# Kernel tuning notes

Hardware: AMD Instinct MI355X
Metric: run time of the kernel (lower is better)

The kernel has to match this reference:

```python
import jax, jax.numpy as jnp
import numpy as np
import math

B, M, DM = 4, 4096, 1024
H, HD = 16, 64            # head_dim = hidden_dim // num_heads
SEG, DIL = 128, 2         # segment_size, dilation_rate
BLOCK_M = 64              # kernel query-block size (min(64, M))
SCALE = HD ** -0.5


def _hilbert_map(seq_len):
    # Faithful port of create_hilbert_mapping_fixed (boustrophedon scan).
    if seq_len <= 64:
        return np.arange(seq_len, dtype=np.int32)
    g = int(math.ceil(math.sqrt(seq_len)))
    mp = np.zeros(seq_len, dtype=np.int64)
    idx = 0
    for row in range(g):
        cols = range(g) if row % 2 == 0 else range(g - 1, -1, -1)
        for col in cols:
            if idx < seq_len:
                lp = row * g + col
                if lp < seq_len:
                    mp[lp] = idx
                    idx += 1
    for i in range(seq_len):
        if i >= idx:
            mp[i] = i
    return mp.astype(np.int32)


def setup_inputs() -> dict:
    key = jax.random.key(0)
    k1, k2, k3 = jax.random.split(key, 3)
    x = jax.random.normal(k1, (B, M, DM), jnp.float32)
    Wqkv = jax.random.normal(k2, (3 * DM, DM), jnp.float32) * 0.02
    Wout = jax.random.normal(k3, (DM, DM), jnp.float32) * 0.02
    hmap = jnp.asarray(_hilbert_map(M))
    return {"x": x, "Wqkv": Wqkv, "Wout": Wout, "hmap": hmap}


def _hilbert_attention(x, Wqkv, Wout, hmap):
    Bn, Mn, _ = x.shape
    qkv = x @ Wqkv.T                                   # [B,M,3*DM]
    qkv = qkv.reshape(Bn, Mn, 3, H, HD).transpose(2, 0, 3, 1, 4)
    q, k, v = qkv[0], qkv[1], qkv[2]                   # [B,H,M,HD]

    S = Mn // SEG           # number of segments
    T = SEG // DIL          # keys per segment (dilated offsets 0, DIL, 2*DIL, ...)
    NB = SEG // BLOCK_M     # query blocks per segment

    # Queries gathered through Hilbert map, pre-scaled (as in kernel).
    qh = q[:, :, hmap, :] * SCALE                      # [B,H,M,HD]

    # Dilated key positions per segment, gathered through Hilbert map.
    key_pos = (jnp.arange(S)[:, None] * SEG + jnp.arange(T)[None, :] * DIL).reshape(-1)
    kh = k[:, :, hmap[key_pos], :].reshape(Bn, H, S, T, HD)
    vh = v[:, :, hmap[key_pos], :].reshape(Bn, H, S, T, HD)

    # Scores per (query-block within segment, key): [B,H,S,NB,BLOCK_M,T]
    qs = qh.reshape(Bn, H, S, NB, BLOCK_M, HD)
    scores = jnp.einsum('bhsnqd,bhstd->bhsnqt', qs, kh)

    # Kernel quirk (faithful): per-KEY max taken over the 64-query block,
    # exp accumulated without rescaling -> NOT a true softmax.
    c = jnp.max(scores, axis=4, keepdims=True)         # max over query block
    w = jnp.exp(scores - c)
    num = jnp.einsum('bhsnqt,bhstd->bhsnqd', w, vh)
    den = 1e-10 + jnp.sum(w, axis=-1, keepdims=True)
    out = (num / den).reshape(Bn, H, Mn, HD)

    # Stored at linear (non-Hilbert) positions, then merged heads + out proj.
    out = out.transpose(0, 2, 1, 3).reshape(Bn, Mn, H * HD)
    return out @ Wout.T


def reference(x, Wqkv, Wout, hmap):
    return _hilbert_attention(x, Wqkv, Wout, hmap)
```

## Files before the change

kernel.cpp:

```cpp
#include <hip/hip_runtime.h>
#include <hip/hip_bf16.h>

#define BB 4
#define MM 4096
#define DM 1024
#define NH 16
#define HDIM 64
#define SEGSZ 128
#define NSEG 32
#define ROWS (BB*MM)
#define QKVC (3*DM)
#define KVROWS (BB*MM/2)
#define KVLD 2048
#define NX4  (ROWS*DM/4)
#define NW14 (QKVC*DM/4)
#define NW24 (DM*DM/4)

typedef __attribute__((ext_vector_type(8))) short bf16x8;
typedef __attribute__((ext_vector_type(4))) float f32x4;

__device__ inline unsigned short f2bf(float f) {
  __hip_bfloat16 h = __float2bfloat16(f);
  return *reinterpret_cast<unsigned short*>(&h);
}

__device__ __forceinline__ void gld16(const ushort* g, ushort* l) {
  __builtin_amdgcn_global_load_lds(
      (const __attribute__((address_space(1))) unsigned int*)g,
      (__attribute__((address_space(3))) unsigned int*)l,
      16, 0, 0);
}

__global__ __launch_bounds__(256) void cvt_all(const float4* __restrict__ x,
                                               const float4* __restrict__ w1,
                                               const float4* __restrict__ w2,
                                               ushort4* __restrict__ xo,
                                               ushort4* __restrict__ w1o,
                                               ushort4* __restrict__ w2o) {
  int i = blockIdx.x * 256 + threadIdx.x;
  const float4* src; ushort4* dst; int off;
  if (i < NX4)              { src = x;  dst = xo;  off = i; }
  else if (i < NX4 + NW14)  { src = w1; dst = w1o; off = i - NX4; }
  else                      { src = w2; dst = w2o; off = i - NX4 - NW14; }
  float4 v = src[off];
  ushort4 o;
  o.x = f2bf(v.x); o.y = f2bf(v.y); o.z = f2bf(v.z); o.w = f2bf(v.w);
  dst[off] = o;
}

#define STAGE_AB(T, KH, DB) do {                                             \
    gld16(pA0 + (T) * 64 + (KH) * 32,                                        \
          sAB + ((DB) * 2 + (KH)) * 8192 + wave * 512);                      \
    gld16(pA1 + (T) * 64 + (KH) * 32,                                        \
          sAB + ((DB) * 2 + (KH)) * 8192 + 4096 + wave * 512);               \
    gld16(pB0 + (T) * 64 + (KH) * 32,                                        \
          sAB + 32768 + ((DB) * 2 + (KH)) * 8192 + wave * 512);              \
    gld16(pB1 + (T) * 64 + (KH) * 32,                                        \
          sAB + 32768 + ((DB) * 2 + (KH)) * 8192 + 4096 + wave * 512);       \
  } while (0)
#define VM4 asm volatile("s_waitcnt vmcnt(4)" ::: "memory")
#define VM0 asm volatile("s_waitcnt vmcnt(0)" ::: "memory")
#define NOPS ((void)0)

#define PH_M(TB, KH, STAGE, VMA) do {                                        \
    const ushort* Ab = sAB + ((TB) * 2 + (KH)) * 8192;                       \
    const ushort* Bb = sAB + 32768 + ((TB) * 2 + (KH)) * 8192;               \
    _Pragma("unroll")                                                        \
    for (int mf = 0; mf < 8; ++mf) {                                         \
      int r = wm * 128 + mf * 16 + m16;                                      \
      af[mf] = *(const bf16x8*)(Ab + r * 32 + ((quad ^ ((r >> 1) & 3)) << 3)); \
    }                                                                        \
    _Pragma("unroll")                                                        \
    for (int nf = 0; nf < 4; ++nf) {                                         \
      int r = wn * 64 + nf * 16 + m16;                                       \
      bfv[nf] = *(const bf16x8*)(Bb + r * 32 + ((quad ^ ((r >> 1) & 3)) << 3)); \
    }                                                                        \
    STAGE; VMA;                                                              \
    __builtin_amdgcn_s_barrier();                                            \
    __builtin_amdgcn_s_setprio(1);                                           \
    _Pragma("unroll")                                                        \
    for (int mf = 0; mf < 8; ++mf)                                           \
      _Pragma("unroll")                                                      \
      for (int nf = 0; nf < 4; ++nf)                                         \
        acc[mf][nf] = __builtin_amdgcn_mfma_f32_16x16x32_bf16(               \
            af[mf], bfv[nf], acc[mf][nf], 0, 0, 0);                          \
    __builtin_amdgcn_s_setprio(0);                                           \
  } while (0)

#define KLOOP_1024                                                           \
  STAGE_AB(0, 0, 0);                                                         \
  STAGE_AB(0, 1, 0);                                                         \
  VM4;                                                                       \
  __builtin_amdgcn_s_barrier();                                              \
  _Pragma("unroll 1")                                                        \
  for (int i = 0; i < 7; ++i) {                                              \
    const int t1 = 2 * i + 1, t2 = 2 * i + 2;                                \
    PH_M(0, 0, STAGE_AB(t1, 0, 1), VM4);                                     \
    PH_M(0, 1, STAGE_AB(t1, 1, 1), VM4);                                     \
    PH_M(1, 0, STAGE_AB(t2, 0, 0), VM4);                                     \
    PH_M(1, 1, STAGE_AB(t2, 1, 0), VM4);                                     \
  }                                                                          \
  PH_M(0, 0, STAGE_AB(15, 0, 1), VM4);                                       \
  PH_M(0, 1, STAGE_AB(15, 1, 1), VM4);                                       \
  PH_M(1, 0, NOPS, VM0);                                                     \
  PH_M(1, 1, NOPS, NOPS);

__global__ __launch_bounds__(512) void gemm_qkv(const ushort* __restrict__ xbf,
                                                const ushort* __restrict__ wqkv,
                                                ushort* __restrict__ qhb,
                                                ushort* __restrict__ kvb,
                                                const int* __restrict__ hmap) {
  __shared__ __align__(16) ushort sAB[65536];
  __shared__ int sRow[256];

  const int blk = blockIdx.x;
  const int tid = threadIdx.x;
  const int lane = tid & 63;
  const int wave = tid >> 6;
  const int m16 = lane & 15;
  const int quad = lane >> 4;
  const int wm = wave >> 2;
  const int wn = wave & 3;

  const int j0 = blk & 255;
  const int swz = (j0 & 7) * 32 + (j0 >> 3);

  const ushort* Bmat; ushort* C; int row0, col0, N;
  if (blk < 256) {
    row0 = (swz >> 2) * 256; col0 = (swz & 3) * 256;
    Bmat = wqkv; C = qhb; N = DM;
  } else {
    row0 = (swz >> 3) * 256; col0 = (swz & 7) * 256;
    Bmat = wqkv + (size_t)DM * DM; C = kvb; N = KVLD;
  }

  if (tid < 256) {
    int m = row0 + tid, xrow;
    if (blk < 256) {
      int b = m >> 12, p = m & 4095;
      xrow = (b << 12) + hmap[p];
    } else {
      int b = m >> 11, idx = m & 2047;
      int ss = idx >> 6, tt = idx & 63;
      xrow = (b << 12) + hmap[ss * SEGSZ + 2 * tt];
    }
    sRow[tid] = xrow;
  }
  __syncthreads();

  const int f0 = wave * 64 + lane, f1 = 512 + f0;
  const int r0 = f0 >> 2, c0 = (f0 & 3) ^ ((f0 >> 3) & 3);
  const int r1 = f1 >> 2, c1 = (f1 & 3) ^ ((f1 >> 3) & 3);
  const ushort* pA0 = xbf + (size_t)sRow[r0] * DM + c0 * 8;
  const ushort* pA1 = xbf + (size_t)sRow[r1] * DM + c1 * 8;
  const ushort* pB0 = Bmat + (size_t)(col0 + r0) * DM + c0 * 8;
  const ushort* pB1 = Bmat + (size_t)(col0 + r1) * DM + c1 * 8;

  f32x4 acc[8][4] = {};
  bf16x8 af[8], bfv[4];

  KLOOP_1024

#pragma unroll
  for (int mf = 0; mf < 8; ++mf)
#pragma unroll
    for (int rr = 0; rr < 4; ++rr) {
      int row = row0 + wm * 128 + mf * 16 + quad * 4 + rr;
#pragma unroll
      for (int nf = 0; nf < 4; ++nf)
        C[(size_t)row * N + col0 + wn * 64 + nf * 16 + m16] = f2bf(acc[mf][nf][rr]);
    }
}

__global__ __launch_bounds__(512) void gemm_out(const ushort* __restrict__ A,
                                                const ushort* __restrict__ Bmat,
                                                float* __restrict__ C) {
  __shared__ __align__(16) ushort sAB[65536];

  const int tid = threadIdx.x;
  const int lane = tid & 63;
  const int wave = tid >> 6;
  const int m16 = lane & 15;
  const int quad = lane >> 4;
  const int wm = wave >> 2;
  const int wn = wave & 3;

  const int j0 = blockIdx.x;
  const int swz = (j0 & 7) * 32 + (j0 >> 3);
  const int row0 = (swz >> 2) * 256;
  const int col0 = (swz & 3) * 256;

  const int f0 = wave * 64 + lane, f1 = 512 + f0;
  const int r0 = f0 >> 2, c0 = (f0 & 3) ^ ((f0 >> 3) & 3);
  const int r1 = f1 >> 2, c1 = (f1 & 3) ^ ((f1 >> 3) & 3);
  const ushort* pA0 = A + (size_t)(row0 + r0) * DM + c0 * 8;
  const ushort* pA1 = A + (size_t)(row0 + r1) * DM + c1 * 8;
  const ushort* pB0 = Bmat + (size_t)(col0 + r0) * DM + c0 * 8;
  const ushort* pB1 = Bmat + (size_t)(col0 + r1) * DM + c1 * 8;

  f32x4 acc[8][4] = {};
  bf16x8 af[8], bfv[4];

  KLOOP_1024

#pragma unroll
  for (int mf = 0; mf < 8; ++mf)
#pragma unroll
    for (int rr = 0; rr < 4; ++rr) {
      int row = row0 + wm * 128 + mf * 16 + quad * 4 + rr;
#pragma unroll
      for (int nf = 0; nf < 4; ++nf)
        C[(size_t)row * DM + col0 + wn * 64 + nf * 16 + m16] = acc[mf][nf][rr];
    }
}

#undef KLOOP_1024
#undef PH_M
#undef STAGE_AB
#undef VM4
#undef VM0
#undef NOPS

__global__ __launch_bounds__(256) void attn_kernel(const ushort* __restrict__ qh,
                                                   const ushort* __restrict__ kv,
                                                   ushort* __restrict__ out) {
  __shared__ __align__(16) ushort sQW[128 * 72];
  __shared__ __align__(16) ushort sK[64 * 72];
  __shared__ __align__(16) ushort sVT[64 * 72];
  __shared__ float sCmaxW[4 * 64];
  __shared__ float sDen[128];

  const int bid = blockIdx.x;
  const int s  = bid & 31;
  const int h  = (bid >> 5) & 15;
  const int b  = bid >> 9;
  const int tid = threadIdx.x;
  const int lane = tid & 63;
  const int wave = tid >> 6;
  const int m16 = lane & 15;
  const int quad = lane >> 4;
  const int qb = wave * 32;
  const int hb = wave >> 1;

  {
    const int qr = tid >> 1;
    const int qc = (tid & 1) * 32;
    const ushort* qrow = qh + (size_t)(b * MM + s * SEGSZ + qr) * DM + h * HDIM + qc;
    *(uint4*)(sQW + qr * 72 + qc)      = ((const uint4*)qrow)[0];
    *(uint4*)(sQW + qr * 72 + qc + 8)  = ((const uint4*)qrow)[1];
    *(uint4*)(sQW + qr * 72 + qc + 16) = ((const uint4*)qrow)[2];
    *(uint4*)(sQW + qr * 72 + qc + 24) = ((const uint4*)qrow)[3];

    const int r = tid >> 2;
    const int c = (tid & 3) * 16;
    const ushort* krow = kv + (size_t)(b * (MM/2) + s * 64 + r) * KVLD + h * HDIM + c;
    const ushort* vrow = krow + DM;
    *(uint4*)(sK + r * 72 + c)     = ((const uint4*)krow)[0];
    *(uint4*)(sK + r * 72 + c + 8) = ((const uint4*)krow)[1];
    ushort vv[16];
    *(uint4*)(vv)     = ((const uint4*)vrow)[0];
    *(uint4*)(vv + 8) = ((const uint4*)vrow)[1];
#pragma unroll
    for (int u = 0; u < 16; ++u) sVT[(c + u) * 72 + r] = vv[u];
  }
  __syncthreads();

  f32x4 sc[2][4];
  {
    bf16x8 aq[2][2], bk[4][2];
#pragma unroll
    for (int ks = 0; ks < 2; ++ks) {
#pragma unroll
      for (int ib = 0; ib < 2; ++ib)
        aq[ib][ks] = *(const bf16x8*)(sQW + (qb + ib * 16 + m16) * 72 + ks * 32 + quad * 8);
#pragma unroll
      for (int j = 0; j < 4; ++j)
        bk[j][ks] = *(const bf16x8*)(sK + (j * 16 + m16) * 72 + ks * 32 + quad * 8);
    }
#pragma unroll
    for (int ib = 0; ib < 2; ++ib)
#pragma unroll
      for (int j = 0; j < 4; ++j) {
        f32x4 a = {};
        a = __builtin_amdgcn_mfma_f32_16x16x32_bf16(aq[ib][0], bk[j][0], a, 0, 0, 0);
        a = __builtin_amdgcn_mfma_f32_16x16x32_bf16(aq[ib][1], bk[j][1], a, 0, 0, 0);
        sc[ib][j] = a * 0.125f;
      }
  }

#pragma unroll
  for (int j = 0; j < 4; ++j) {
    float m = -1e30f;
#pragma unroll
    for (int ib = 0; ib < 2; ++ib)
#pragma unroll
      for (int r = 0; r < 4; ++r) m = fmaxf(m, sc[ib][j][r]);
    m = fmaxf(m, __shfl_xor(m, 16));
    m = fmaxf(m, __shfl_xor(m, 32));
    if (quad == 0) sCmaxW[wave * 64 + j * 16 + m16] = m;
  }
  __syncthreads();

  {
    float part[2][4] = {};
#pragma unroll
    for (int j = 0; j < 4; ++j) {
      const int col = j * 16 + m16;
      float c0 = fmaxf(sCmaxW[hb * 128 + col], sCmaxW[hb * 128 + 64 + col]);
#pragma unroll
      for (int ib = 0; ib < 2; ++ib)
#pragma unroll
        for (int r = 0; r < 4; ++r) {
          float ww = __expf(sc[ib][j][r] - c0);
          sc[ib][j][r] = ww;
          part[ib][r] += ww;
        }
    }
#pragma unroll
    for (int ib = 0; ib < 2; ++ib)
#pragma unroll
      for (int r = 0; r < 4; ++r) {
        float p = part[ib][r];
        p += __shfl_xor(p, 1); p += __shfl_xor(p, 2);
        p += __shfl_xor(p, 4); p += __shfl_xor(p, 8);
        if (m16 == 0) sDen[qb + ib * 16 + quad * 4 + r] = p;
      }
#pragma unroll
    for (int ib = 0; ib < 2; ++ib)
#pragma unroll
      for (int j = 0; j < 4; ++j)
#pragma unroll
        for (int r = 0; r < 4; ++r)
          sQW[(qb + ib * 16 + quad * 4 + r) * 72 + j * 16 + m16] = f2bf(sc[ib][j][r]);
  }
  __syncthreads();

  f32x4 o[2][4] = {};
  {
    bf16x8 aw[2][2], bv[4][2];
#pragma unroll
    for (int ks = 0; ks < 2; ++ks) {
#pragma unroll
      for (int ib = 0; ib < 2; ++ib)
        aw[ib][ks] = *(const bf16x8*)(sQW + (qb + ib * 16 + m16) * 72 + ks * 32 + quad * 8);
#pragma unroll
      for (int j = 0; j < 4; ++j)
        bv[j][ks] = *(const bf16x8*)(sVT + (j * 16 + m16) * 72 + ks * 32 + quad * 8);
    }
#pragma unroll
    for (int ib = 0; ib < 2; ++ib)
#pragma unroll
      for (int j = 0; j < 4; ++j) {
        o[ib][j] = __builtin_amdgcn_mfma_f32_16x16x32_bf16(aw[ib][0], bv[j][0], o[ib][j], 0, 0, 0);
        o[ib][j] = __builtin_amdgcn_mfma_f32_16x16x32_bf16(aw[ib][1], bv[j][1], o[ib][j], 0, 0, 0);
      }
  }

#pragma unroll
  for (int ib = 0; ib < 2; ++ib)
#pragma unroll
    for (int r = 0; r < 4; ++r) {
      const int lrow = qb + ib * 16 + quad * 4 + r;
      float rd = 1.0f / (1e-10f + sDen[lrow]);
      ushort* op = out + (size_t)(b * MM + s * SEGSZ + lrow) * DM + h * HDIM + m16;
#pragma unroll
      for (int j = 0; j < 4; ++j)
        op[j * 16] = f2bf(o[ib][j][r] * rd);
    }
}

extern "C" void kernel_launch(void* const* d_in, const int* in_sizes, int n_in,
                              void* d_out, int out_size, void* d_ws, size_t ws_size,
                              hipStream_t stream) {
  const float* x    = (const float*)d_in[0];
  const float* wqkv = (const float*)d_in[1];
  const float* wout = (const float*)d_in[2];
  const int*   hmap = (const int*)d_in[3];
  float* outp = (float*)d_out;

  ushort* xbf    = (ushort*)d_ws;
  ushort* wqkvbf = xbf + (size_t)ROWS * DM;
  ushort* woutbf = wqkvbf + (size_t)QKVC * DM;
  ushort* qhb    = woutbf + (size_t)DM * DM;
  ushort* kvb    = qhb + (size_t)ROWS * DM;
  ushort* attn   = kvb + (size_t)KVROWS * KVLD;

  cvt_all<<<(NX4 + NW14 + NW24 + 255) / 256, 256, 0, stream>>>(
      (const float4*)x, (const float4*)wqkv, (const float4*)wout,
      (ushort4*)xbf, (ushort4*)wqkvbf, (ushort4*)woutbf);

  gemm_qkv<<<512, 512, 0, stream>>>(xbf, wqkvbf, qhb, kvb, hmap);

  attn_kernel<<<BB * NH * NSEG, 256, 0, stream>>>(qhb, kvb, attn);

  gemm_out<<<256, 512, 0, stream>>>(attn, woutbf, outp);
}
```

Measured before the change: 252.2 us.

## Split QKV GEMM phases into half-N sub-phases with deeper prefetch pipeline

The QKV projection GEMM main loop now splits each k-phase into two half-width sub-phases, each issuing half of the B fragment loads and half the MFMAs, with A and B global-to-LDS staging interleaved separately. Prefetch runs three stages ahead instead of two, with finer vmcnt waits. The goal is to overlap memory latency better and reduce register pressure (bfv shrinks from 4 to 2 fragments). In exchange there are twice as many barriers per k-step and A fragments are reused across sub-phases. The output GEMM keeps the original schedule under renamed macros.

```diff
diff --git a/kernel.cpp b/kernel.cpp
--- a/kernel.cpp
+++ b/kernel.cpp
@@ -48,62 +48,93 @@
   dst[off] = o;
 }
 
-#define STAGE_AB(T, KH, DB) do {                                             \
+#define QSTAGE_A(T, KH, DB) do {                                             \
     gld16(pA0 + (T) * 64 + (KH) * 32,                                        \
           sAB + ((DB) * 2 + (KH)) * 8192 + wave * 512);                      \
     gld16(pA1 + (T) * 64 + (KH) * 32,                                        \
           sAB + ((DB) * 2 + (KH)) * 8192 + 4096 + wave * 512);               \
+  } while (0)
+#define QSTAGE_B(T, KH, DB) do {                                             \
     gld16(pB0 + (T) * 64 + (KH) * 32,                                        \
           sAB + 32768 + ((DB) * 2 + (KH)) * 8192 + wave * 512);              \
     gld16(pB1 + (T) * 64 + (KH) * 32,                                        \
           sAB + 32768 + ((DB) * 2 + (KH)) * 8192 + 4096 + wave * 512);       \
   } while (0)
-#define VM4 asm volatile("s_waitcnt vmcnt(4)" ::: "memory")
-#define VM0 asm volatile("s_waitcnt vmcnt(0)" ::: "memory")
-#define NOPS ((void)0)
-
-#define PH_M(TB, KH, STAGE, VMA) do {                                        \
-    const ushort* Ab = sAB + ((TB) * 2 + (KH)) * 8192;                       \
-    const ushort* Bb = sAB + 32768 + ((TB) * 2 + (KH)) * 8192;               \
+#define QVM6 asm volatile("s_waitcnt vmcnt(6)" ::: "memory")
+#define QVM8 asm volatile("s_waitcnt vmcnt(8)" ::: "memory")
+#define QVM0 asm volatile("s_waitcnt vmcnt(0)" ::: "memory")
+#define QNOPS ((void)0)
+
+#define QPH_TAIL(CH)                                                         \
+    __builtin_amdgcn_s_barrier();                                            \
+    __builtin_amdgcn_s_setprio(1);                                           \
+    _Pragma("unroll")                                                        \
+    for (int mf = 0; mf < 8; ++mf)                                           \
+      _Pragma("unroll")                                                      \
+      for (int nf = 0; nf < 2; ++nf)                                         \
+        acc[mf][(CH) * 2 + nf] = __builtin_amdgcn_mfma_f32_16x16x32_bf16(    \
+            af[mf], bfv[nf], acc[mf][(CH) * 2 + nf], 0, 0, 0);               \
+    __builtin_amdgcn_s_setprio(0);
+
+#define QPH_F_B(AB, BB_, STAGE, VMA) do {                                    \
+    const ushort* Ab = (AB); const ushort* Bb = (BB_);                       \
     _Pragma("unroll")                                                        \
     for (int mf = 0; mf < 8; ++mf) {                                         \
       int r = wm * 128 + mf * 16 + m16;                                      \
       af[mf] = *(const bf16x8*)(Ab + r * 32 + ((quad ^ ((r >> 1) & 3)) << 3)); \
     }                                                                        \
     _Pragma("unroll")                                                        \
-    for (int nf = 0; nf < 4; ++nf) {                                         \
+    for (int nf = 0; nf < 2; ++nf) {                                         \
       int r = wn * 64 + nf * 16 + m16;                                       \
       bfv[nf] = *(const bf16x8*)(Bb + r * 32 + ((quad ^ ((r >> 1) & 3)) << 3)); \
     }                                                                        \
     STAGE; VMA;                                                              \
-    __builtin_amdgcn_s_barrier();                                            \
-    __builtin_amdgcn_s_setprio(1);                                           \
-    _Pragma("unroll")                                                        \
-    for (int mf = 0; mf < 8; ++mf)                                           \
-      _Pragma("unroll")                                                      \
-      for (int nf = 0; nf < 4; ++nf)                                         \
-        acc[mf][nf] = __builtin_amdgcn_mfma_f32_16x16x32_bf16(               \
-            af[mf], bfv[nf], acc[mf][nf], 0, 0, 0);                          \
-    __builtin_amdgcn_s_setprio(0);                                           \
-  } while (0)
-
-#define KLOOP_1024                                                           \
-  STAGE_AB(0, 0, 0);                                                         \
-  STAGE_AB(0, 1, 0);                                                         \
-  VM4;                                                                       \
+    QPH_TAIL(0)                                                              \
+  } while (0)
+
+#define QPH_L_B(BB_, STAGE, VMA) do {                                        \
+    const ushort* Bb = (BB_);                                                \
+    _Pragma("unroll")                                                        \
+    for (int nf = 0; nf < 2; ++nf) {                                         \
+      int r = wn * 64 + 32 + nf * 16 + m16;                                  \
+      bfv[nf] = *(const bf16x8*)(Bb + r * 32 + ((quad ^ ((r >> 1) & 3)) << 3)); \
+    }                                                                        \
+    STAGE; VMA;                                                              \
+    QPH_TAIL(1)                                                              \
+  } while (0)
+
+#define QPH_F(TB, KH, STAGE, VMA) \
+    QPH_F_B(sAB + ((TB) * 2 + (KH)) * 8192, sAB + 32768 + ((TB) * 2 + (KH)) * 8192, STAGE, VMA)
+#define QPH_L(TB, KH, STAGE, VMA) \
+    QPH_L_B(sAB + 32768 + ((TB) * 2 + (KH)) * 8192, STAGE, VMA)
+
+#define QKLOOP_1024                                                          \
+  QSTAGE_A(0, 0, 0); QSTAGE_B(0, 0, 0);                                      \
+  QSTAGE_A(0, 1, 0); QSTAGE_B(0, 1, 0);                                      \
+  QSTAGE_A(1, 0, 1); QSTAGE_B(1, 0, 1);                                      \
+  QVM8;                                                                      \
   __builtin_amdgcn_s_barrier();                                              \
   _Pragma("unroll 1")                                                        \
   for (int i = 0; i < 7; ++i) {                                              \
-    const int t1 = 2 * i + 1, t2 = 2 * i + 2;                                \
-    PH_M(0, 0, STAGE_AB(t1, 0, 1), VM4);                                     \
-    PH_M(0, 1, STAGE_AB(t1, 1, 1), VM4);                                     \
-    PH_M(1, 0, STAGE_AB(t2, 0, 0), VM4);                                     \
-    PH_M(1, 1, STAGE_AB(t2, 1, 0), VM4);                                     \
+    const int t1 = 2 * i + 1, t2 = 2 * i + 2, t3 = 2 * i + 3;                \
+    QPH_F(0, 0, QSTAGE_A(t1, 1, 1), QNOPS);                                  \
+    QPH_L(0, 0, QSTAGE_B(t1, 1, 1), QVM6);                                   \
+    QPH_F(0, 1, QSTAGE_A(t2, 0, 0), QNOPS);                                  \
+    QPH_L(0, 1, QSTAGE_B(t2, 0, 0), QVM6);                                   \
+    QPH_F(1, 0, QSTAGE_A(t2, 1, 0), QNOPS);                                  \
+    QPH_L(1, 0, QSTAGE_B(t2, 1, 0), QVM6);                                   \
+    QPH_F(1, 1, QSTAGE_A(t3, 0, 1), QNOPS);                                  \
+    QPH_L(1, 1, QSTAGE_B(t3, 0, 1), QVM6);                                   \
   }                                                                          \
-  PH_M(0, 0, STAGE_AB(15, 0, 1), VM4);                                       \
-  PH_M(0, 1, STAGE_AB(15, 1, 1), VM4);                                       \
-  PH_M(1, 0, NOPS, VM0);                                                     \
-  PH_M(1, 1, NOPS, NOPS);
+  QPH_F(0, 0, QSTAGE_A(15, 1, 1), QNOPS);                                    \
+  QPH_L(0, 0, QSTAGE_B(15, 1, 1), QVM0);                                     \
+  _Pragma("unroll 1")                                                        \
+  for (int u = 1; u < 4; ++u) {                                              \
+    const ushort* AbU = sAB + u * 8192;                                      \
+    const ushort* BbU = sAB + 32768 + u * 8192;                              \
+    QPH_F_B(AbU, BbU, QNOPS, QNOPS);                                         \
+    QPH_L_B(BbU, QNOPS, QNOPS);                                              \
+  }
 
 __global__ __launch_bounds__(512) void gemm_qkv(const ushort* __restrict__ xbf,
                                                 const ushort* __restrict__ wqkv,
@@ -157,9 +188,9 @@
   const ushort* pB1 = Bmat + (size_t)(col0 + r1) * DM + c1 * 8;
 
   f32x4 acc[8][4] = {};
-  bf16x8 af[8], bfv[4];
-
-  KLOOP_1024
+  bf16x8 af[8], bfv[2];
+
+  QKLOOP_1024
 
 #pragma unroll
   for (int mf = 0; mf < 8; ++mf)
@@ -171,6 +202,76 @@
         C[(size_t)row * N + col0 + wn * 64 + nf * 16 + m16] = f2bf(acc[mf][nf][rr]);
     }
 }
+
+#undef QKLOOP_1024
+#undef QPH_F
+#undef QPH_L
+#undef QPH_F_B
+#undef QPH_L_B
+#undef QPH_TAIL
+#undef QSTAGE_A
+#undef QSTAGE_B
+#undef QVM6
+#undef QVM8
+#undef QVM0
+#undef QNOPS
+
+#define OSTAGE_AB(T, KH, DB) do {                                            \
+    gld16(pA0 + (T) * 64 + (KH) * 32,                                        \
+          sAB + ((DB) * 2 + (KH)) * 8192 + wave * 512);                      \
+    gld16(pA1 + (T) * 64 + (KH) * 32,                                        \
+          sAB + ((DB) * 2 + (KH)) * 8192 + 4096 + wave * 512);               \
+    gld16(pB0 + (T) * 64 + (KH) * 32,                                        \
+          sAB + 32768 + ((DB) * 2 + (KH)) * 8192 + wave * 512);              \
+    gld16(pB1 + (T) * 64 + (KH) * 32,                                        \
+          sAB + 32768 + ((DB) * 2 + (KH)) * 8192 + 4096 + wave * 512);       \
+  } while (0)
+#define OVM4 asm volatile("s_waitcnt vmcnt(4)" ::: "memory")
+#define OVM0 asm volatile("s_waitcnt vmcnt(0)" ::: "memory")
+#define ONOPS ((void)0)
+
+#define OPH_M(TB, KH, STAGE, VMA) do {                                       \
+    const ushort* Ab = sAB + ((TB) * 2 + (KH)) * 8192;                       \
+    const ushort* Bb = sAB + 32768 + ((TB) * 2 + (KH)) * 8192;               \
+    _Pragma("unroll")                                                        \
+    for (int mf = 0; mf < 8; ++mf) {                                         \
+      int r = wm * 128 + mf * 16 + m16;                                      \
+      af[mf] = *(const bf16x8*)(Ab + r * 32 + ((quad ^ ((r >> 1) & 3)) << 3)); \
+    }                                                                        \
+    _Pragma("unroll")                                                        \
+    for (int nf = 0; nf < 4; ++nf) {                                         \
+      int r = wn * 64 + nf * 16 + m16;                                       \
+      bfv[nf] = *(const bf16x8*)(Bb + r * 32 + ((quad ^ ((r >> 1) & 3)) << 3)); \
+    }                                                                        \
+    STAGE; VMA;                                                              \
+    __builtin_amdgcn_s_barrier();                                            \
+    __builtin_amdgcn_s_setprio(1);                                           \
+    _Pragma("unroll")                                                        \
+    for (int mf = 0; mf < 8; ++mf)                                           \
+      _Pragma("unroll")                                                      \
+      for (int nf = 0; nf < 4; ++nf)                                         \
+        acc[mf][nf] = __builtin_amdgcn_mfma_f32_16x16x32_bf16(               \
+            af[mf], bfv[nf], acc[mf][nf], 0, 0, 0);                          \
+    __builtin_amdgcn_s_setprio(0);                                           \
+  } while (0)
+
+#define OKLOOP_1024                                                          \
+  OSTAGE_AB(0, 0, 0);                                                        \
+  OSTAGE_AB(0, 1, 0);                                                        \
+  OVM4;                                                                      \
+  __builtin_amdgcn_s_barrier();                                              \
+  _Pragma("unroll 1")                                                        \
+  for (int i = 0; i < 7; ++i) {                                              \
+    const int t1 = 2 * i + 1, t2 = 2 * i + 2;                                \
+    OPH_M(0, 0, OSTAGE_AB(t1, 0, 1), OVM4);                                  \
+    OPH_M(0, 1, OSTAGE_AB(t1, 1, 1), OVM4);                                  \
+    OPH_M(1, 0, OSTAGE_AB(t2, 0, 0), OVM4);                                  \
+    OPH_M(1, 1, OSTAGE_AB(t2, 1, 0), OVM4);                                  \
+  }                                                                          \
+  OPH_M(0, 0, OSTAGE_AB(15, 0, 1), OVM4);                                    \
+  OPH_M(0, 1, OSTAGE_AB(15, 1, 1), OVM4);                                    \
+  OPH_M(1, 0, ONOPS, OVM0);                                                  \
+  OPH_M(1, 1, ONOPS, ONOPS);
 
 __global__ __launch_bounds__(512) void gemm_out(const ushort* __restrict__ A,
                                                 const ushort* __restrict__ Bmat,
@@ -201,7 +302,7 @@
   f32x4 acc[8][4] = {};
   bf16x8 af[8], bfv[4];
 
-  KLOOP_1024
+  OKLOOP_1024
 
 #pragma unroll
   for (int mf = 0; mf < 8; ++mf)
@@ -214,12 +315,12 @@
     }
 }
 
-#undef KLOOP_1024
-#undef PH_M
-#undef STAGE_AB
-#undef VM4
-#undef VM0
-#undef NOPS
+#undef OKLOOP_1024
+#undef OPH_M
+#undef OSTAGE_AB
+#undef OVM4
+#undef OVM0
+#undef ONOPS
 
 __global__ __launch_bounds__(256) void attn_kernel(const ushort* __restrict__ qh,
                                                    const ushort* __restrict__ kv,
```

Result: slower. 261.9 us, median of 2 (+3.8%).
